# Performance work log

Measured on AMD Instinct MI355X. Metric: run time of the kernel, lower is better.

The kernel has to match this reference:

```python
import jax, jax.numpy as jnp
import numpy as np
from jax import lax

DT = 0.05          # constructor dt
TAU_DC = 50.0      # constructor tau_dc (ema mode)
ALPHA = DT / max(TAU_DC, 1e-6)


def setup_inputs() -> dict:
    key = jax.random.key(0)
    B, T, F = 16, 4096, 512
    x = jax.random.normal(key, (B, T, F), dtype=jnp.float32)
    return {
        "input_current": x,
        "vb_t": jnp.zeros((F,), jnp.float32),        # vb = 0.0 per feature
        "A_t": jnp.ones((F,), jnp.float32),          # A = 1.0
        "th_t": jnp.ones((F,), jnp.float32),         # theta = 1.0
        "gain_t": jnp.ones((F,), jnp.float32),       # input_gain = 1.0
        "tref_t": jnp.full((F,), 2.0, jnp.float32),
    }


def reference(input_current, vb_t, A_t, th_t, gain_t, tref_t):
    B, T, F = input_current.shape
    # refractory length in steps, clamp >= 1 (ceil(tau_ref/dt))
    ref_steps = jnp.maximum(jnp.ceil(tref_t / max(DT, 1e-6)), 1.0).astype(jnp.int32)  # [F]

    xs = jnp.moveaxis(input_current, 1, 0)  # [T, B, F]

    def step(carry, inp):
        refc, ema = carry            # refc: [B,F] int32, ema: [B,F] float
        xt_raw, t = inp
        xt = xt_raw * gain_t         # scaled input
        # EMA baseline; at t==0 (reset_states) the EMA is initialized to xt
        ema = jnp.where(t == 0, xt, ema + ALPHA * (xt - ema))
        va_cand = vb_t - A_t * (xt - ema)            # amplifier (noise_std == 0)
        in_ref = refc > 0
        fired = (~in_ref) & (jnp.abs(va_cand - vb_t) >= th_t)
        va_next = jnp.where(in_ref | fired, vb_t, va_cand)
        refc = jnp.where(in_ref, refc - 1, refc)
        refc = jnp.where(fired, ref_steps, refc)
        return (refc, ema), (va_next, fired)

    refc0 = jnp.zeros((B, F), jnp.int32)
    ema0 = jnp.zeros((B, F), input_current.dtype)
    _, (va_seq, fired_seq) = lax.scan(step, (refc0, ema0), (xs, jnp.arange(T)))

    # va_trace[:,0,:] = vb, va_trace[:,t+1,:] = va_next_t
    va_trace = jnp.concatenate(
        [jnp.broadcast_to(vb_t, (B, 1, F)), jnp.moveaxis(va_seq, 0, 1)], axis=1
    )  # [B, T+1, F]
    fired_b = jnp.moveaxis(fired_seq, 0, 1)  # [B, T, F]
    spikes = jnp.concatenate([fired_b, fired_b[:, -1:, :]], axis=1)  # [B, T+1, F] bool
    return va_trace, spikes
```

## Files before the change

### kernel.cpp

```cpp
#include <hip/hip_runtime.h>
#include <stdint.h>


#define L_CHUNK 256
#define TS 64
#define DEPTH 4
#define K2_UNROLL 8

typedef const __attribute__((address_space(1))) uint32_t* gptr_t;
typedef __attribute__((address_space(3))) uint32_t* lptr_t;

__global__ __launch_bounds__(64, 1)
void fa_scan_kernel(const float* __restrict__ x,
                    const float* __restrict__ vb,
                    const float* __restrict__ A,
                    const float* __restrict__ th,
                    const float* __restrict__ gain,
                    const float* __restrict__ tref,
                    float* __restrict__ emas,
                    int*   __restrict__ nrs,
                    int B, int T, int F) {
#pragma clang fp contract(off)
    __shared__ float lds[DEPTH][TS][64];
    const int lane = threadIdx.x;
    const int gpb = F >> 6;
    const int bi = blockIdx.x;
    const int b = bi / gpb;
    const int f0 = (bi - b * gpb) << 6;
    const int f = f0 + lane;
    const int i = b * F + f;
    const int N = B * F;

    const float vbf = vb[f], Af = A[f], thf = th[f], gf = gain[f];
    const float alpha = 0.001f;
    const int rs = (int)fmaxf(ceilf(tref[f] / 0.05f), 1.0f);

    const float* xb = x + (size_t)b * T * F + f0;
    const float* gsrc0 = xb + (size_t)(lane >> 4) * F + ((lane & 15) << 2);
    const int ntiles = T / TS;

#define ISSUE_TILE(J)                                                         \
    do {                                                                      \
        const float* s_ = gsrc0 + (size_t)(J) * TS * F;                       \
        float* d_ = &lds[(J) & (DEPTH - 1)][0][0];                            \
        _Pragma("unroll")                                                     \
        for (int jj = 0; jj < 16; ++jj) {                                     \
            __builtin_amdgcn_global_load_lds(                                 \
                (gptr_t)(s_ + (size_t)(4 * jj) * F),                          \
                (lptr_t)(d_ + 4 * jj * 64), 16, 0, 0);                        \
        }                                                                     \
    } while (0)

    ISSUE_TILE(0);
    ISSUE_TILE(1);
    ISSUE_TILE(2);

    bool fastAll = __all((gf == 1.0f) && (Af == 1.0f) && (vbf == 0.0f));

    float ema = 0.0f;
    int nr = 0;

    for (int k = 0; k < ntiles; ++k) {
        if (k < ntiles - 2)       asm volatile("s_waitcnt vmcnt(32)" ::: "memory");
        else if (k == ntiles - 2) asm volatile("s_waitcnt vmcnt(16)" ::: "memory");
        else                      asm volatile("s_waitcnt vmcnt(0)"  ::: "memory");
        __builtin_amdgcn_sched_barrier(0);

        const int slot = k & (DEPTH - 1);

        if (k == 0) {
            float x0 = lds[0][0][lane];
            ema = fastAll ? x0 : (x0 * gf);
        } else if ((k & 3) == 0) {
            int c = k >> 2;
            emas[(size_t)c * N + i] = ema;
            nrs[(size_t)c * N + i] = nr + k * TS;
        }

        float ra[8], rb[8];
#pragma unroll
        for (int j = 0; j < 8; ++j) ra[j] = lds[slot][j][lane];

        if (fastAll) {
#pragma unroll
            for (int t8 = 0; t8 < TS / 8; ++t8) {
                if (t8 < TS / 8 - 1) {
#pragma unroll
                    for (int j = 0; j < 8; ++j)
                        rb[j] = lds[slot][(t8 + 1) * 8 + j][lane];
                }
#pragma unroll
                for (int j = 0; j < 8; ++j) {
                    const int t = t8 * 8 + j;
                    float xv = ra[j];
                    float d1 = xv - ema;
                    float am = alpha * d1;
                    ema = ema + am;
                    float d2 = xv - ema;
                    bool cross = fabsf(d2) >= thf;
                    bool tge = t >= nr;
                    bool fired = cross && tge;
                    nr = fired ? (t + 1 + rs) : nr;
                }
#pragma unroll
                for (int j = 0; j < 8; ++j) ra[j] = rb[j];
            }
        } else {
#pragma unroll
            for (int t8 = 0; t8 < TS / 8; ++t8) {
                if (t8 < TS / 8 - 1) {
#pragma unroll
                    for (int j = 0; j < 8; ++j)
                        rb[j] = lds[slot][(t8 + 1) * 8 + j][lane];
                }
#pragma unroll
                for (int j = 0; j < 8; ++j) {
                    const int t = t8 * 8 + j;
                    float xt = ra[j] * gf;
                    float d1 = xt - ema;
                    float am = alpha * d1;
                    ema = ema + am;
                    float d2 = xt - ema;
                    float av = Af * d2;
                    float vc = vbf - av;
                    float dv = vc - vbf;
                    bool cross = fabsf(dv) >= thf;
                    bool tge = t >= nr;
                    bool fired = cross && tge;
                    nr = fired ? (t + 1 + rs) : nr;
                }
#pragma unroll
                for (int j = 0; j < 8; ++j) ra[j] = rb[j];
            }
        }
        nr -= TS;

        if (k + 3 < ntiles) ISSUE_TILE(k + 3);
    }
#undef ISSUE_TILE
}

__global__ __launch_bounds__(256)
void fa_emit_kernel(const float* __restrict__ x,
                    const float* __restrict__ vb,
                    const float* __restrict__ A,
                    const float* __restrict__ th,
                    const float* __restrict__ gain,
                    const float* __restrict__ tref,
                    const float* __restrict__ emas,
                    const int*   __restrict__ nrs,
                    float* __restrict__ out,
                    int B, int T, int F, int nchunks) {
#pragma clang fp contract(off)
    int N = B * F;
    int tid = blockIdx.x * blockDim.x + threadIdx.x;
    if (tid >= N * nchunks) return;
    int i = tid % N;
    int k = tid / N;
    int f = i % F;
    int b = i / F;
    const float vbf = vb[f], Af = A[f], thf = th[f], gf = gain[f];
    const float alpha = 0.001f;
    int rs = (int)fmaxf(ceilf(tref[f] / 0.05f), 1.0f);

    const float* xp = x + (size_t)b * T * F + f;
    float* va_out   = out + (size_t)b * (T + 1) * F + f;
    float* sp_out   = out + (size_t)B * (T + 1) * F + (size_t)b * (T + 1) * F + f;

    int tbeg = k * L_CHUNK;
    int tend = tbeg + L_CHUNK;
    if (tend > T) tend = T;

    float cur[K2_UNROLL], nxt[K2_UNROLL];
#pragma unroll
    for (int u = 0; u < K2_UNROLL; ++u) cur[u] = xp[(size_t)(tbeg + u) * F];

    float ema;
    int nr;
    if (k == 0) {
        ema = cur[0] * gf;
        nr = 0;
        va_out[0] = vbf;
    } else {
        ema = emas[(size_t)k * N + i];
        nr = nrs[(size_t)k * N + i];
    }

    float last_sp = 0.0f;
    for (int t0 = tbeg; t0 < tend; t0 += K2_UNROLL) {
        if (t0 + K2_UNROLL < tend) {
#pragma unroll
            for (int u = 0; u < K2_UNROLL; ++u)
                nxt[u] = xp[(size_t)(t0 + K2_UNROLL + u) * F];
        }
#pragma unroll
        for (int u = 0; u < K2_UNROLL; ++u) {
            int t = t0 + u;
            float xt = cur[u] * gf;
            float d1 = xt - ema;
            float am = alpha * d1;
            ema = ema + am;
            float d2 = xt - ema;
            float av = Af * d2;
            float vc = vbf - av;
            float dv = vc - vbf;
            bool cross = fabsf(dv) >= thf;
            bool tge = t >= nr;
            bool fired = cross && tge;
            float va_next = (cross || !tge) ? vbf : vc;
            nr = fired ? (t + 1 + rs) : nr;
            float spv = fired ? 1.0f : 0.0f;
            va_out[(size_t)(t + 1) * F] = va_next;
            sp_out[(size_t)t * F] = spv;
            last_sp = spv;
        }
#pragma unroll
        for (int u = 0; u < K2_UNROLL; ++u) cur[u] = nxt[u];
    }
    if (tend == T) sp_out[(size_t)T * F] = last_sp;
}

__global__ __launch_bounds__(64, 1)
void fa_neuron_mono(const float* __restrict__ x,
                    const float* __restrict__ vb,
                    const float* __restrict__ A,
                    const float* __restrict__ th,
                    const float* __restrict__ gain,
                    const float* __restrict__ tref,
                    float* __restrict__ out,
                    int B, int T, int F) {
#pragma clang fp contract(off)
    int tid = blockIdx.x * blockDim.x + threadIdx.x;
    if (tid >= B * F) return;
    int f = tid % F;
    int b = tid / F;
    const float vbf = vb[f], Af = A[f], thf = th[f], gf = gain[f];
    const float alpha = 0.001f;
    int rs = (int)fmaxf(ceilf(tref[f] / 0.05f), 1.0f);
    const float* xp = x + (size_t)b * T * F + f;
    float* va_out   = out + (size_t)b * (T + 1) * F + f;
    float* sp_out   = out + (size_t)B * (T + 1) * F + (size_t)b * (T + 1) * F + f;
    va_out[0] = vbf;
    float ema = 0.0f;
    int nr = 0;
    for (int t = 0; t < T; ++t) {
        float xt = xp[(size_t)t * F] * gf;
        if (t == 0) {
            ema = xt;
        } else {
            float d1 = xt - ema;
            float am = alpha * d1;
            ema = ema + am;
        }
        float d2 = xt - ema;
        float av = Af * d2;
        float vc = vbf - av;
        float dv = vc - vbf;
        bool cross = fabsf(dv) >= thf;
        bool tge = t >= nr;
        bool fired = cross && tge;
        float va_next = (cross || !tge) ? vbf : vc;
        nr = fired ? (t + 1 + rs) : nr;
        float spv = fired ? 1.0f : 0.0f;
        va_out[(size_t)(t + 1) * F] = va_next;
        sp_out[(size_t)t * F] = spv;
        if (t == T - 1) sp_out[(size_t)T * F] = spv;
    }
}

extern "C" void kernel_launch(void* const* d_in, const int* in_sizes, int n_in,
                              void* d_out, int out_size, void* d_ws, size_t ws_size,
                              hipStream_t stream) {
    const float* x    = (const float*)d_in[0];
    const float* vb   = (const float*)d_in[1];
    const float* A    = (const float*)d_in[2];
    const float* th   = (const float*)d_in[3];
    const float* gain = (const float*)d_in[4];
    const float* tref = (const float*)d_in[5];
    float* out = (float*)d_out;

    int F = in_sizes[1];
    long long BF = (long long)out_size / 2 - in_sizes[0];
    int B = (int)(BF / F);
    int T = (int)(in_sizes[0] / BF);
    int N = B * F;

    int nchunks = (T + L_CHUNK - 1) / L_CHUNK;
    size_t ws_need = (size_t)nchunks * N * (sizeof(float) + sizeof(int));

    bool tiled_ok = (ws_size >= ws_need) && (T % L_CHUNK == 0) &&
                    (T % TS == 0) && (T / TS >= 4) && (F % 64 == 0) &&
                    (L_CHUNK == 4 * TS);

    if (!tiled_ok) {
        int block = 64;
        int grid = (N + block - 1) / block;
        fa_neuron_mono<<<grid, block, 0, stream>>>(x, vb, A, th, gain, tref, out, B, T, F);
        return;
    }

    float* emas = (float*)d_ws;
    int*   nrs  = (int*)(emas + (size_t)nchunks * N);

    {
        int block = 64;
        int grid = N / 64;
        fa_scan_kernel<<<grid, block, 0, stream>>>(x, vb, A, th, gain, tref,
                                                   emas, nrs, B, T, F);
    }
    {
        int total = N * nchunks;
        int block = 256;
        int grid = (total + block - 1) / block;
        fa_emit_kernel<<<grid, block, 0, stream>>>(x, vb, A, th, gain, tref,
                                                   emas, nrs, out, B, T, F, nchunks);
    }
}
```

Baseline: 178.1 us.

## Interleave two batch rows per wavefront in scan kernel for ILP

Each scan wavefront now processes two independent batch rows (p and p+B/2) for the same 64 features. Their EMA/refractory recurrences are interleaved so the two serial dependency chains can overlap. The grid is halved and the LDS buffer doubled, with the prefetch lookahead reduced from three tiles to two to fit. This trades wavefront count for per-wave instruction-level parallelism, which could leave more CUs idle since the grid was already small. A B%2 guard is added to the tiled path.

```diff
diff --git a/kernel.cpp b/kernel.cpp
--- a/kernel.cpp
+++ b/kernel.cpp
@@ -21,121 +21,170 @@
                     int*   __restrict__ nrs,
                     int B, int T, int F) {
 #pragma clang fp contract(off)
-    __shared__ float lds[DEPTH][TS][64];
+    __shared__ float lds[DEPTH][2][TS][64];
     const int lane = threadIdx.x;
     const int gpb = F >> 6;
+    const int halfB = B >> 1;
     const int bi = blockIdx.x;
-    const int b = bi / gpb;
-    const int f0 = (bi - b * gpb) << 6;
-    const int f = f0 + lane;
-    const int i = b * F + f;
+    const int p = bi / gpb;
+    const int g = bi - p * gpb;
+    const int f = (g << 6) + lane;
+    const int b0 = p, b1 = p + halfB;
+    const int i0 = b0 * F + f;
+    const int i1 = b1 * F + f;
     const int N = B * F;
 
     const float vbf = vb[f], Af = A[f], thf = th[f], gf = gain[f];
     const float alpha = 0.001f;
     const int rs = (int)fmaxf(ceilf(tref[f] / 0.05f), 1.0f);
 
-    const float* xb = x + (size_t)b * T * F + f0;
-    const float* gsrc0 = xb + (size_t)(lane >> 4) * F + ((lane & 15) << 2);
+    const size_t lane_off = (size_t)(lane >> 4) * F + ((lane & 15) << 2);
+    const float* g0 = x + (size_t)b0 * T * F + (size_t)(g << 6) + lane_off;
+    const float* g1 = x + (size_t)b1 * T * F + (size_t)(g << 6) + lane_off;
     const int ntiles = T / TS;
 
 #define ISSUE_TILE(J)                                                         \
     do {                                                                      \
-        const float* s_ = gsrc0 + (size_t)(J) * TS * F;                       \
-        float* d_ = &lds[(J) & (DEPTH - 1)][0][0];                            \
+        const float* sa_ = g0 + (size_t)(J) * TS * F;                         \
+        const float* sb_ = g1 + (size_t)(J) * TS * F;                         \
+        float* da_ = &lds[(J) & (DEPTH - 1)][0][0][0];                        \
+        float* db_ = &lds[(J) & (DEPTH - 1)][1][0][0];                        \
         _Pragma("unroll")                                                     \
-        for (int jj = 0; jj < 16; ++jj) {                                     \
+        for (int jj = 0; jj < 16; ++jj)                                       \
             __builtin_amdgcn_global_load_lds(                                 \
-                (gptr_t)(s_ + (size_t)(4 * jj) * F),                          \
-                (lptr_t)(d_ + 4 * jj * 64), 16, 0, 0);                        \
-        }                                                                     \
+                (gptr_t)(sa_ + (size_t)(4 * jj) * F),                         \
+                (lptr_t)(da_ + 4 * jj * 64), 16, 0, 0);                       \
+        _Pragma("unroll")                                                     \
+        for (int jj = 0; jj < 16; ++jj)                                       \
+            __builtin_amdgcn_global_load_lds(                                 \
+                (gptr_t)(sb_ + (size_t)(4 * jj) * F),                         \
+                (lptr_t)(db_ + 4 * jj * 64), 16, 0, 0);                       \
     } while (0)
 
     ISSUE_TILE(0);
     ISSUE_TILE(1);
-    ISSUE_TILE(2);
 
     bool fastAll = __all((gf == 1.0f) && (Af == 1.0f) && (vbf == 0.0f));
 
-    float ema = 0.0f;
-    int nr = 0;
+    float ema0 = 0.0f, ema1 = 0.0f;
+    int nr0 = 0, nr1 = 0;
 
     for (int k = 0; k < ntiles; ++k) {
-        if (k < ntiles - 2)       asm volatile("s_waitcnt vmcnt(32)" ::: "memory");
-        else if (k == ntiles - 2) asm volatile("s_waitcnt vmcnt(16)" ::: "memory");
-        else                      asm volatile("s_waitcnt vmcnt(0)"  ::: "memory");
+        if (k < ntiles - 1) asm volatile("s_waitcnt vmcnt(32)" ::: "memory");
+        else                asm volatile("s_waitcnt vmcnt(0)"  ::: "memory");
         __builtin_amdgcn_sched_barrier(0);
 
         const int slot = k & (DEPTH - 1);
 
         if (k == 0) {
-            float x0 = lds[0][0][lane];
-            ema = fastAll ? x0 : (x0 * gf);
+            float xa = lds[0][0][0][lane];
+            float xb = lds[0][1][0][lane];
+            ema0 = fastAll ? xa : (xa * gf);
+            ema1 = fastAll ? xb : (xb * gf);
         } else if ((k & 3) == 0) {
             int c = k >> 2;
-            emas[(size_t)c * N + i] = ema;
-            nrs[(size_t)c * N + i] = nr + k * TS;
-        }
-
-        float ra[8], rb[8];
-#pragma unroll
-        for (int j = 0; j < 8; ++j) ra[j] = lds[slot][j][lane];
+            emas[(size_t)c * N + i0] = ema0;
+            nrs[(size_t)c * N + i0] = nr0 + k * TS;
+            emas[(size_t)c * N + i1] = ema1;
+            nrs[(size_t)c * N + i1] = nr1 + k * TS;
+        }
+
+        float ra0[8], rb0[8], ra1[8], rb1[8];
+#pragma unroll
+        for (int j = 0; j < 8; ++j) {
+            ra0[j] = lds[slot][0][j][lane];
+            ra1[j] = lds[slot][1][j][lane];
+        }
 
         if (fastAll) {
 #pragma unroll
             for (int t8 = 0; t8 < TS / 8; ++t8) {
                 if (t8 < TS / 8 - 1) {
 #pragma unroll
-                    for (int j = 0; j < 8; ++j)
-                        rb[j] = lds[slot][(t8 + 1) * 8 + j][lane];
+                    for (int j = 0; j < 8; ++j) {
+                        rb0[j] = lds[slot][0][(t8 + 1) * 8 + j][lane];
+                        rb1[j] = lds[slot][1][(t8 + 1) * 8 + j][lane];
+                    }
                 }
 #pragma unroll
                 for (int j = 0; j < 8; ++j) {
                     const int t = t8 * 8 + j;
-                    float xv = ra[j];
-                    float d1 = xv - ema;
-                    float am = alpha * d1;
-                    ema = ema + am;
-                    float d2 = xv - ema;
-                    bool cross = fabsf(d2) >= thf;
-                    bool tge = t >= nr;
-                    bool fired = cross && tge;
-                    nr = fired ? (t + 1 + rs) : nr;
+                    {
+                        float xv = ra0[j];
+                        float d1 = xv - ema0;
+                        float am = alpha * d1;
+                        ema0 = ema0 + am;
+                        float d2 = xv - ema0;
+                        bool cross = fabsf(d2) >= thf;
+                        bool tge = t >= nr0;
+                        bool fired = cross && tge;
+                        nr0 = fired ? (t + 1 + rs) : nr0;
+                    }
+                    {
+                        float xv = ra1[j];
+                        float d1 = xv - ema1;
+                        float am = alpha * d1;
+                        ema1 = ema1 + am;
+                        float d2 = xv - ema1;
+                        bool cross = fabsf(d2) >= thf;
+                        bool tge = t >= nr1;
+                        bool fired = cross && tge;
+                        nr1 = fired ? (t + 1 + rs) : nr1;
+                    }
                 }
 #pragma unroll
-                for (int j = 0; j < 8; ++j) ra[j] = rb[j];
+                for (int j = 0; j < 8; ++j) { ra0[j] = rb0[j]; ra1[j] = rb1[j]; }
             }
         } else {
 #pragma unroll
             for (int t8 = 0; t8 < TS / 8; ++t8) {
                 if (t8 < TS / 8 - 1) {
 #pragma unroll
-                    for (int j = 0; j < 8; ++j)
-                        rb[j] = lds[slot][(t8 + 1) * 8 + j][lane];
+                    for (int j = 0; j < 8; ++j) {
+                        rb0[j] = lds[slot][0][(t8 + 1) * 8 + j][lane];
+                        rb1[j] = lds[slot][1][(t8 + 1) * 8 + j][lane];
+                    }
                 }
 #pragma unroll
                 for (int j = 0; j < 8; ++j) {
                     const int t = t8 * 8 + j;
-                    float xt = ra[j] * gf;
-                    float d1 = xt - ema;
-                    float am = alpha * d1;
-                    ema = ema + am;
-                    float d2 = xt - ema;
-                    float av = Af * d2;
-                    float vc = vbf - av;
-                    float dv = vc - vbf;
-                    bool cross = fabsf(dv) >= thf;
-                    bool tge = t >= nr;
-                    bool fired = cross && tge;
-                    nr = fired ? (t + 1 + rs) : nr;
+                    {
+                        float xt = ra0[j] * gf;
+                        float d1 = xt - ema0;
+                        float am = alpha * d1;
+                        ema0 = ema0 + am;
+                        float d2 = xt - ema0;
+                        float av = Af * d2;
+                        float vc = vbf - av;
+                        float dv = vc - vbf;
+                        bool cross = fabsf(dv) >= thf;
+                        bool tge = t >= nr0;
+                        bool fired = cross && tge;
+                        nr0 = fired ? (t + 1 + rs) : nr0;
+                    }
+                    {
+                        float xt = ra1[j] * gf;
+                        float d1 = xt - ema1;
+                        float am = alpha * d1;
+                        ema1 = ema1 + am;
+                        float d2 = xt - ema1;
+                        float av = Af * d2;
+                        float vc = vbf - av;
+                        float dv = vc - vbf;
+                        bool cross = fabsf(dv) >= thf;
+                        bool tge = t >= nr1;
+                        bool fired = cross && tge;
+                        nr1 = fired ? (t + 1 + rs) : nr1;
+                    }
                 }
 #pragma unroll
-                for (int j = 0; j < 8; ++j) ra[j] = rb[j];
+                for (int j = 0; j < 8; ++j) { ra0[j] = rb0[j]; ra1[j] = rb1[j]; }
             }
         }
-        nr -= TS;
-
-        if (k + 3 < ntiles) ISSUE_TILE(k + 3);
+        nr0 -= TS;
+        nr1 -= TS;
+
+        if (k + 2 < ntiles) ISSUE_TILE(k + 2);
     }
 #undef ISSUE_TILE
 }
@@ -290,7 +339,7 @@
 
     bool tiled_ok = (ws_size >= ws_need) && (T % L_CHUNK == 0) &&
                     (T % TS == 0) && (T / TS >= 4) && (F % 64 == 0) &&
-                    (L_CHUNK == 4 * TS);
+                    (B % 2 == 0) && (L_CHUNK == 4 * TS);
 
     if (!tiled_ok) {
         int block = 64;
@@ -304,7 +353,7 @@
 
     {
         int block = 64;
-        int grid = N / 64;
+        int grid = (B / 2) * (F / 64);
         fa_scan_kernel<<<grid, block, 0, stream>>>(x, vb, A, th, gain, tref,
                                                    emas, nrs, B, T, F);
     }
```

Result: slower. 254.4 us (+42.8%).
